# Kernel tuning notes

Measured on AMD Instinct MI355X. Metric: run time of the kernel, lower is better.

The kernel has to match this reference:

```python
import jax, jax.numpy as jnp
import numpy as np

B, C, H, W = 64, 128, 32, 32
GROUPS = 32
EPS = 1e-6
SCALE = 0.044194173824159216  # 1/sqrt(512), as hardcoded in the torch module


def setup_inputs() -> dict:
    key = jax.random.key(0)
    ks = jax.random.split(key, 12)
    s = 1.0 / np.sqrt(C)
    return {
        "x": jax.random.normal(ks[0], (B, C, H, W), dtype=jnp.float32),
        "gn_w": jax.random.normal(ks[1], (C,), dtype=jnp.float32) * 0.02 + 1.0,
        "gn_b": jax.random.normal(ks[2], (C,), dtype=jnp.float32) * 0.02,
        "wq": jax.random.uniform(ks[3], (C, C), jnp.float32, -s, s),
        "bq": jax.random.uniform(ks[4], (C,), jnp.float32, -s, s),
        "wk": jax.random.uniform(ks[5], (C, C), jnp.float32, -s, s),
        "bk": jax.random.uniform(ks[6], (C,), jnp.float32, -s, s),
        "wv": jax.random.uniform(ks[7], (C, C), jnp.float32, -s, s),
        "bv": jax.random.uniform(ks[8], (C,), jnp.float32, -s, s),
        "wo": jax.random.uniform(ks[9], (C, C), jnp.float32, -s, s),
        "bo": jax.random.uniform(ks[10], (C,), jnp.float32, -s, s),
    }


def reference(x, gn_w, gn_b, wq, bq, wk, bk, wv, bv, wo, bo):
    b = x.shape[0]
    res = x
    # GroupNorm(32 groups, 128 channels): normalize over (channels_per_group, H, W)
    xg = x.reshape(b, GROUPS, C // GROUPS, H * W)
    mean = xg.mean(axis=(2, 3), keepdims=True)
    var = xg.var(axis=(2, 3), keepdims=True)
    xn = (xg - mean) * jax.lax.rsqrt(var + EPS)
    xn = xn.reshape(b, C, H, W) * gn_w[:, None, None] + gn_b[:, None, None]
    # flatten spatial -> sequence: [b, S=1024, C=128]
    t = xn.reshape(b, C, H * W).transpose(0, 2, 1)
    q = t @ wq.T + bq
    k = t @ wk.T + bk
    v = t @ wv.T + bv
    att = jnp.einsum('bsc,btc->bst', q, k) * SCALE  # [b, S, S]
    att = jax.nn.softmax(att, axis=-1)
    o = jnp.einsum('bst,btc->bsc', att, v)
    o = o @ wo.T + bo
    out = o.transpose(0, 2, 1).reshape(b, C, H, W) + res
    return out
```

## Files before the change

kernel.cpp:

```cpp
#include <hip/hip_runtime.h>
#include <hip/hip_bf16.h>

#define BATCH 64
#define CCH 128
#define SEQ 1024
#define NG 32
#define EPSV 1e-6f
#define SCALEV 0.044194173824159216f
#define QPRE (0.044194173824159216f * 1.4426950408889634f)

typedef short v8s __attribute__((ext_vector_type(8)));
typedef short v4s __attribute__((ext_vector_type(4)));
typedef float v4f __attribute__((ext_vector_type(4)));
typedef int   v4i __attribute__((ext_vector_type(4)));
typedef unsigned short us;

__device__ __forceinline__ us f2bf(float f) {
    __hip_bfloat16 h = __float2bfloat16(f);
    return *reinterpret_cast<us*>(&h);
}

__device__ __forceinline__ int cvtpk(float lo, float hi) {
    int r;
    asm("v_cvt_pk_bf16_f32 %0, %1, %2" : "=v"(r) : "v"(lo), "v"(hi));
    return r;
}

#if __has_builtin(__builtin_amdgcn_exp2f)
#define EXP2F(x) __builtin_amdgcn_exp2f(x)
#else
#define EXP2F(x) exp2f(x)
#endif

#define MFMA16(a, b, c) __builtin_amdgcn_mfma_f32_16x16x32_bf16(a, b, c, 0, 0, 0)

__device__ __forceinline__ void gld_lds16(const us* g, us* l) {
    __builtin_amdgcn_global_load_lds(
        (const __attribute__((address_space(1))) void*)g,
        (__attribute__((address_space(3))) void*)l, 16, 0, 0);
}

__global__ void prep_gn(const float* __restrict__ wq, const float* __restrict__ wk,
                        const float* __restrict__ wv, const float* __restrict__ wo,
                        us* wbf, const float* __restrict__ x,
                        float* meanr, float* rstdr) {
    int tid = threadIdx.x;
    if (blockIdx.x < 256) {
        int i = blockIdx.x * 256 + tid;
        const float* srcs[4] = {wq, wk, wv, wo};
        wbf[i] = f2bf(srcs[i >> 14][i & 16383]);
        return;
    }
    int bg = blockIdx.x - 256;
    const float4* p = (const float4*)(x + (size_t)bg * (4 * SEQ));
    float s1 = 0.f, s2 = 0.f;
    #pragma unroll
    for (int i = 0; i < 4; i++) {
        float4 v = p[i * 256 + tid];
        s1 += v.x + v.y + v.z + v.w;
        s2 += v.x * v.x + v.y * v.y + v.z * v.z + v.w * v.w;
    }
    #pragma unroll
    for (int off = 32; off; off >>= 1) {
        s1 += __shfl_down(s1, off);
        s2 += __shfl_down(s2, off);
    }
    __shared__ float a1[4], a2[4];
    int w = tid >> 6, l = tid & 63;
    if (l == 0) { a1[w] = s1; a2[w] = s2; }
    __syncthreads();
    if (tid == 0) {
        float t1 = a1[0] + a1[1] + a1[2] + a1[3];
        float t2 = a2[0] + a2[1] + a2[2] + a2[3];
        float mean = t1 * (1.0f / (4 * SEQ));
        float var  = t2 * (1.0f / (4 * SEQ)) - mean * mean;
        meanr[bg] = mean;
        rstdr[bg] = rsqrtf(var + EPSV);
    }
}

__global__ __launch_bounds__(256, 4) void qkv_kernel(
    const float* __restrict__ x, const float* __restrict__ gn_w,
    const float* __restrict__ gn_b, const float* __restrict__ meanr,
    const float* __restrict__ rstdr, const us* __restrict__ wbf,
    const float* __restrict__ bq, const float* __restrict__ bk,
    const float* __restrict__ bv,
    us* Q, us* K, us* Vt)
{
    __shared__ us tls[64 * 136];
    __shared__ float sa[CCH], sb[CCH];
    int b  = blockIdx.x >> 4;
    int s0 = (blockIdx.x & 15) * 64;
    int tid = threadIdx.x;
    const float* xb = x + (size_t)b * CCH * SEQ;

    if (tid < CCH) {
        int g = tid >> 2;
        float rs = rstdr[b * NG + g];
        float mu = meanr[b * NG + g];
        float a_ = rs * gn_w[tid];
        sa[tid] = a_;
        sb[tid] = gn_b[tid] - mu * a_;
    }
    __syncthreads();

    #pragma unroll
    for (int rep = 0; rep < 8; rep++) {
        int idx = rep * 256 + tid;
        int c = idx >> 4, s4 = idx & 15;
        float4 v = *(const float4*)&xb[c * SEQ + s0 + s4 * 4];
        float a_ = sa[c], b_ = sb[c];
        int sbase = s4 * 4;
        tls[(sbase + 0) * 136 + c] = f2bf(v.x * a_ + b_);
        tls[(sbase + 1) * 136 + c] = f2bf(v.y * a_ + b_);
        tls[(sbase + 2) * 136 + c] = f2bf(v.z * a_ + b_);
        tls[(sbase + 3) * 136 + c] = f2bf(v.w * a_ + b_);
    }
    __syncthreads();

    int w = tid >> 6, lane = tid & 63;
    int m = lane & 15, quad = lane >> 4;

    v8s a[4][4];
    #pragma unroll
    for (int st = 0; st < 4; st++)
        #pragma unroll
        for (int ch = 0; ch < 4; ch++)
            a[st][ch] = *(const v8s*)&tls[(st * 16 + m) * 136 + ch * 32 + quad * 8];

    us* Qb = Q + (size_t)b * SEQ * CCH;
    us* Kb = K + (size_t)b * SEQ * CCH;
    us* Vb = Vt + (size_t)b * CCH * SEQ;

    #pragma unroll
    for (int t = 0; t < 6; t++) {
        int T = w * 6 + t;
        int o = T >> 3, ct = T & 7;
        int col = ct * 16 + m;
        const us* wmat = wbf + o * 16384;
        v8s bfr[4];
        #pragma unroll
        for (int ch = 0; ch < 4; ch++)
            bfr[ch] = *(const v8s*)&wmat[(ct * 16 + m) * 128 + ch * 32 + quad * 8];
        const float* bb = (o == 0) ? bq : (o == 1) ? bk : bv;
        float bias = bb[col];

        #pragma unroll
        for (int st = 0; st < 4; st++) {
            v4f acc = {0,0,0,0};
            #pragma unroll
            for (int ch = 0; ch < 4; ch++)
                acc = MFMA16(a[st][ch], bfr[ch], acc);
            int srow = s0 + st * 16 + quad * 4;
            if (o == 0) {
                #pragma unroll
                for (int r = 0; r < 4; r++)
                    Qb[(size_t)(srow + r) * 128 + col] = f2bf((acc[r] + bias) * QPRE);
            } else if (o == 1) {
                #pragma unroll
                for (int r = 0; r < 4; r++)
                    Kb[(size_t)(srow + r) * 128 + col] = f2bf(acc[r] + bias);
            } else {
                v4s pk;
                #pragma unroll
                for (int r = 0; r < 4; r++) pk[r] = (short)f2bf(acc[r] + bias);
                *(v4s*)&Vb[(size_t)col * SEQ + srow] = pk;
            }
        }
    }
}

__global__ __launch_bounds__(256, 2) void attn_kernel(
    const us* __restrict__ Q, const us* __restrict__ K,
    const us* __restrict__ Vt, const us* __restrict__ wbo,
    const float* __restrict__ bo, const float* __restrict__ x,
    float* __restrict__ out)
{
    __shared__ char smem_raw[65536];

    int i = blockIdx.x;
    int b  = (i & 7) * 8 + ((i >> 3) & 7);
    int qt = i >> 6;
    int tid = threadIdx.x;
    int w = tid >> 6, lane = tid & 63;
    int m = lane & 15, quad = lane >> 4;
    int qrow0 = qt * 128 + w * 32;
    const us* Qb = Q + (size_t)b * SEQ * CCH;
    const us* Kb = K + (size_t)b * SEQ * CCH;
    const us* Vb = Vt + (size_t)b * CCH * SEQ;

    v8s aq[2][4];
    #pragma unroll
    for (int st = 0; st < 2; st++)
        #pragma unroll
        for (int ch = 0; ch < 4; ch++)
            aq[st][ch] = *(const v8s*)&Qb[(size_t)(qrow0 + st * 16 + m) * 128 + ch * 32 + quad * 8];

    v4f oacc[2][8];
    #pragma unroll
    for (int st = 0; st < 2; st++)
        #pragma unroll
        for (int ct = 0; ct < 8; ct++) oacc[st][ct] = (v4f){0, 0, 0, 0};
    float lrun[2] = {0.f, 0.f};

    const us* kg[4]; const us* vg[4];
    int jb = w * 4;
    #pragma unroll
    for (int j4 = 0; j4 < 4; j4++) {
        int j = jb + j4;
        int kr = 4 * j + (lane >> 4);
        kg[j4] = Kb + (size_t)kr * 128 + ((lane & 15) ^ (kr & 15)) * 8;
        int vc = 8 * j + (lane >> 3);
        vg[j4] = Vb + (size_t)vc * SEQ + ((lane & 7) ^ (vc & 7)) * 8;
    }
    int idx0 = 2 * (quad & 1) * 16 + m;
    int idx1 = idx0 + 16;

    #pragma unroll
    for (int j4 = 0; j4 < 4; j4++) {
        gld_lds16(kg[j4], (us*)smem_raw + (jb + j4) * 512);
        gld_lds16(vg[j4], (us*)(smem_raw + 16384) + (jb + j4) * 512);
    }

    for (int kt = 0; kt < 16; kt++) {
        int boff  = (kt & 1) ? 32768 : 0;
        int boffn = boff ^ 32768;
        __builtin_amdgcn_s_barrier();
        if (kt < 15) {
            #pragma unroll
            for (int j4 = 0; j4 < 4; j4++) {
                gld_lds16(kg[j4] + (size_t)(kt + 1) * 8192,
                          (us*)(smem_raw + boffn) + (jb + j4) * 512);
                gld_lds16(vg[j4] + (size_t)(kt + 1) * 64,
                          (us*)(smem_raw + boffn + 16384) + (jb + j4) * 512);
            }
            asm volatile("s_waitcnt vmcnt(8)" ::: "memory");
        } else {
            asm volatile("s_waitcnt vmcnt(0)" ::: "memory");
        }
        __builtin_amdgcn_s_barrier();

        const us* kl = (const us*)(smem_raw + boff);
        const us* vl = (const us*)(smem_raw + boff + 16384);

        __builtin_amdgcn_s_setprio(1);

        v4f acc0[4], acc1[4];
        int e[2][4][2];

        #define QK_STEP(c2) { \
            int krow = (c2) * 16 + m; \
            v4f A0 = {0,0,0,0}, A1 = {0,0,0,0}; \
            _Pragma("unroll") \
            for (int ch = 0; ch < 4; ch++) { \
                int chunk = (ch * 4 + quad) ^ (krow & 15); \
                v8s kb = *(const v8s*)&kl[krow * 128 + chunk * 8]; \
                A0 = MFMA16(kb, aq[0][ch], A0); \
                A1 = MFMA16(kb, aq[1][ch], A1); \
            } \
            acc0[c2] = A0; acc1[c2] = A1; }

        #define EXP_STEP(c2) { \
            float p0[4], p1[4]; \
            _Pragma("unroll") \
            for (int r = 0; r < 4; r++) { \
                p0[r] = EXP2F(acc0[c2][r]); \
                p1[r] = EXP2F(acc1[c2][r]); \
                lrun[0] += p0[r]; lrun[1] += p1[r]; \
            } \
            e[0][c2][0] = cvtpk(p0[0], p0[1]); e[0][c2][1] = cvtpk(p0[2], p0[3]); \
            e[1][c2][0] = cvtpk(p1[0], p1[1]); e[1][c2][1] = cvtpk(p1[2], p1[3]); }

        QK_STEP(0)
        QK_STEP(1)
        EXP_STEP(0)
        QK_STEP(2)
        EXP_STEP(1)
        QK_STEP(3)
        EXP_STEP(2)
        EXP_STEP(3)

        #define SHFL_STEP(kc2, paw) { \
            _Pragma("unroll") \
            for (int st = 0; st < 2; st++) { \
                int c0 = (quad < 2) ? e[st][2 * (kc2)][0] : e[st][2 * (kc2) + 1][0]; \
                int c1 = (quad < 2) ? e[st][2 * (kc2)][1] : e[st][2 * (kc2) + 1][1]; \
                v4i t; \
                t[0] = __shfl(c0, idx0); \
                t[1] = __shfl(c1, idx0); \
                t[2] = __shfl(c0, idx1); \
                t[3] = __shfl(c1, idx1); \
                paw[st] = __builtin_bit_cast(v8s, t); } }

        v8s pa0[2], pa1[2];
        SHFL_STEP(0, pa0)
        #pragma unroll
        for (int ct = 0; ct < 8; ct++) {
            int vrow = ct * 16 + m;
            int chunk = quad ^ (vrow & 7);
            v8s vb = *(const v8s*)&vl[vrow * 64 + chunk * 8];
            oacc[0][ct] = MFMA16(pa0[0], vb, oacc[0][ct]);
            oacc[1][ct] = MFMA16(pa0[1], vb, oacc[1][ct]);
        }
        SHFL_STEP(1, pa1)
        #pragma unroll
        for (int ct = 0; ct < 8; ct++) {
            int vrow = ct * 16 + m;
            int chunk = (4 + quad) ^ (vrow & 7);
            v8s vb = *(const v8s*)&vl[vrow * 64 + chunk * 8];
            oacc[0][ct] = MFMA16(pa1[0], vb, oacc[0][ct]);
            oacc[1][ct] = MFMA16(pa1[1], vb, oacc[1][ct]);
        }
        __builtin_amdgcn_s_setprio(0);
        #undef QK_STEP
        #undef EXP_STEP
        #undef SHFL_STEP
    }

    float inv[2][4];
    #pragma unroll
    for (int st = 0; st < 2; st++) {
        float rs = lrun[st];
        rs += __shfl_xor(rs, 16);
        rs += __shfl_xor(rs, 32);
        #pragma unroll
        for (int r = 0; r < 4; r++)
            inv[st][r] = 1.0f / __shfl(rs, quad * 4 + r);
    }
    __syncthreads();
    us* olds = (us*)smem_raw;
    #pragma unroll
    for (int st = 0; st < 2; st++)
        #pragma unroll
        for (int ct = 0; ct < 8; ct++)
            #pragma unroll
            for (int r = 0; r < 4; r++)
                olds[(w * 32 + st * 16 + quad * 4 + r) * 136 + ct * 16 + m] =
                    f2bf(oacc[st][ct][r] * inv[st][r]);
    __syncthreads();

    const float* xb = x + (size_t)b * CCH * SEQ;
    float* ob = out + (size_t)b * CCH * SEQ;
    int sbase = qt * 128 + w * 32;
    v8s obf[2][4];
    #pragma unroll
    for (int st = 0; st < 2; st++)
        #pragma unroll
        for (int ch = 0; ch < 4; ch++)
            obf[st][ch] = *(const v8s*)&olds[(w * 32 + st * 16 + m) * 136 + ch * 32 + quad * 8];
    #pragma unroll
    for (int mt = 0; mt < 8; mt++) {
        v8s af[4];
        #pragma unroll
        for (int ch = 0; ch < 4; ch++)
            af[ch] = *(const v8s*)&wbo[(mt * 16 + m) * 128 + ch * 32 + quad * 8];
        #pragma unroll
        for (int st = 0; st < 2; st++) {
            v4f acc = {0,0,0,0};
            #pragma unroll
            for (int ch = 0; ch < 4; ch++)
                acc = MFMA16(af[ch], obf[st][ch], acc);
            #pragma unroll
            for (int r = 0; r < 4; r++) {
                int c = mt * 16 + quad * 4 + r;
                int idx = c * SEQ + sbase + st * 16 + m;
                ob[idx] = acc[r] + bo[c] + xb[idx];
            }
        }
    }
}

extern "C" void kernel_launch(void* const* d_in, const int* in_sizes, int n_in,
                              void* d_out, int out_size, void* d_ws, size_t ws_size,
                              hipStream_t stream) {
    const float* x    = (const float*)d_in[0];
    const float* gn_w = (const float*)d_in[1];
    const float* gn_b = (const float*)d_in[2];
    const float* wq   = (const float*)d_in[3];
    const float* bq   = (const float*)d_in[4];
    const float* wk   = (const float*)d_in[5];
    const float* bk   = (const float*)d_in[6];
    const float* wv   = (const float*)d_in[7];
    const float* bv   = (const float*)d_in[8];
    const float* wo   = (const float*)d_in[9];
    const float* bo   = (const float*)d_in[10];
    float* out = (float*)d_out;

    char* ws = (char*)d_ws;
    us* wbf      = (us*)ws;
    float* meanr = (float*)(ws + 131072);
    float* rstdr = (float*)(ws + 139264);
    us* Qbuf     = (us*)(ws + 147456);
    us* Kbuf     = (us*)(ws + 147456 + 16777216ull);
    us* Vtbuf    = (us*)(ws + 147456 + 2ull * 16777216ull);

    prep_gn<<<256 + BATCH * NG, 256, 0, stream>>>(wq, wk, wv, wo, wbf, x, meanr, rstdr);
    qkv_kernel<<<1024, 256, 0, stream>>>(x, gn_w, gn_b, meanr, rstdr, wbf,
                                         bq, bk, bv, Qbuf, Kbuf, Vtbuf);
    attn_kernel<<<512, 256, 0, stream>>>(Qbuf, Kbuf, Vtbuf, wbf + 3 * 16384,
                                         bo, x, out);
}
```

Baseline: 168.1 us.

## Stage QKV outputs through LDS for coalesced stores; single-buffer V to raise attention occupancy

The QKV projection now writes its bf16 results into shared memory per output matrix and then stores them to global memory as coalesced 16-byte vectors, replacing scattered 2-byte stores. The attention kernel keeps K double-buffered but gives V a single 16KB buffer, reloaded after a barrier once the PV step finishes. This drops LDS to 48KB so launch bounds can request 3 blocks per CU. The trade-off is an extra barrier per key tile and less overlap on the V load, which is now exposed to latency.

```diff
diff --git a/kernel.cpp b/kernel.cpp
--- a/kernel.cpp
+++ b/kernel.cpp
@@ -87,7 +87,7 @@
     const float* __restrict__ bv,
     us* Q, us* K, us* Vt)
 {
-    __shared__ us tls[64 * 136];
+    __shared__ us tls[9216];
     __shared__ float sa[CCH], sb[CCH];
     int b  = blockIdx.x >> 4;
     int s0 = (blockIdx.x & 15) * 64;
@@ -127,56 +127,76 @@
         #pragma unroll
         for (int ch = 0; ch < 4; ch++)
             a[st][ch] = *(const v8s*)&tls[(st * 16 + m) * 136 + ch * 32 + quad * 8];
+    __syncthreads();
 
     us* Qb = Q + (size_t)b * SEQ * CCH;
     us* Kb = K + (size_t)b * SEQ * CCH;
     us* Vb = Vt + (size_t)b * CCH * SEQ;
 
     #pragma unroll
-    for (int t = 0; t < 6; t++) {
-        int T = w * 6 + t;
-        int o = T >> 3, ct = T & 7;
-        int col = ct * 16 + m;
+    for (int o = 0; o < 3; o++) {
         const us* wmat = wbf + o * 16384;
-        v8s bfr[4];
-        #pragma unroll
-        for (int ch = 0; ch < 4; ch++)
-            bfr[ch] = *(const v8s*)&wmat[(ct * 16 + m) * 128 + ch * 32 + quad * 8];
         const float* bb = (o == 0) ? bq : (o == 1) ? bk : bv;
-        float bias = bb[col];
-
-        #pragma unroll
-        for (int st = 0; st < 4; st++) {
-            v4f acc = {0,0,0,0};
+        #pragma unroll
+        for (int t2 = 0; t2 < 2; t2++) {
+            int T = (o * 2 + t2) * 4 + w;
+            int ct = T & 7;
+            int col = ct * 16 + m;
+            v8s bfr[4];
             #pragma unroll
             for (int ch = 0; ch < 4; ch++)
-                acc = MFMA16(a[st][ch], bfr[ch], acc);
-            int srow = s0 + st * 16 + quad * 4;
-            if (o == 0) {
+                bfr[ch] = *(const v8s*)&wmat[(ct * 16 + m) * 128 + ch * 32 + quad * 8];
+            float bias = bb[col];
+            #pragma unroll
+            for (int st = 0; st < 4; st++) {
+                v4f acc = {0,0,0,0};
                 #pragma unroll
-                for (int r = 0; r < 4; r++)
-                    Qb[(size_t)(srow + r) * 128 + col] = f2bf((acc[r] + bias) * QPRE);
-            } else if (o == 1) {
-                #pragma unroll
-                for (int r = 0; r < 4; r++)
-                    Kb[(size_t)(srow + r) * 128 + col] = f2bf(acc[r] + bias);
-            } else {
-                v4s pk;
-                #pragma unroll
-                for (int r = 0; r < 4; r++) pk[r] = (short)f2bf(acc[r] + bias);
-                *(v4s*)&Vb[(size_t)col * SEQ + srow] = pk;
+                for (int ch = 0; ch < 4; ch++)
+                    acc = MFMA16(a[st][ch], bfr[ch], acc);
+                if (o < 2) {
+                    #pragma unroll
+                    for (int r = 0; r < 4; r++) {
+                        float v = acc[r] + bias;
+                        if (o == 0) v *= QPRE;
+                        tls[(st * 16 + quad * 4 + r) * 136 + col] = f2bf(v);
+                    }
+                } else {
+                    #pragma unroll
+                    for (int r = 0; r < 4; r++)
+                        tls[col * 72 + st * 16 + quad * 4 + r] = f2bf(acc[r] + bias);
+                }
             }
         }
-    }
-}
-
-__global__ __launch_bounds__(256, 2) void attn_kernel(
+        __syncthreads();
+        if (o < 2) {
+            us* dst = (o == 0) ? Qb : Kb;
+            #pragma unroll
+            for (int rep = 0; rep < 4; rep++) {
+                int idx = rep * 256 + tid;
+                int row = idx >> 4, c8 = idx & 15;
+                *(v8s*)&dst[(size_t)(s0 + row) * 128 + c8 * 8] =
+                    *(const v8s*)&tls[row * 136 + c8 * 8];
+            }
+        } else {
+            #pragma unroll
+            for (int rep = 0; rep < 4; rep++) {
+                int idx = rep * 256 + tid;
+                int c = idx >> 3, c8 = idx & 7;
+                *(v8s*)&Vb[(size_t)c * SEQ + s0 + c8 * 8] =
+                    *(const v8s*)&tls[c * 72 + c8 * 8];
+            }
+        }
+        if (o < 2) __syncthreads();
+    }
+}
+
+__global__ __launch_bounds__(256, 3) void attn_kernel(
     const us* __restrict__ Q, const us* __restrict__ K,
     const us* __restrict__ Vt, const us* __restrict__ wbo,
     const float* __restrict__ bo, const float* __restrict__ x,
     float* __restrict__ out)
 {
-    __shared__ char smem_raw[65536];
+    __shared__ char smem_raw[49152];
 
     int i = blockIdx.x;
     int b  = (i & 7) * 8 + ((i >> 3) & 7);
@@ -219,29 +239,24 @@
     #pragma unroll
     for (int j4 = 0; j4 < 4; j4++) {
         gld_lds16(kg[j4], (us*)smem_raw + (jb + j4) * 512);
-        gld_lds16(vg[j4], (us*)(smem_raw + 16384) + (jb + j4) * 512);
+        gld_lds16(vg[j4], (us*)(smem_raw + 32768) + (jb + j4) * 512);
     }
 
     for (int kt = 0; kt < 16; kt++) {
-        int boff  = (kt & 1) ? 32768 : 0;
-        int boffn = boff ^ 32768;
-        __builtin_amdgcn_s_barrier();
+        int kcur = (kt & 1) ? 16384 : 0;
         if (kt < 15) {
             #pragma unroll
-            for (int j4 = 0; j4 < 4; j4++) {
+            for (int j4 = 0; j4 < 4; j4++)
                 gld_lds16(kg[j4] + (size_t)(kt + 1) * 8192,
-                          (us*)(smem_raw + boffn) + (jb + j4) * 512);
-                gld_lds16(vg[j4] + (size_t)(kt + 1) * 64,
-                          (us*)(smem_raw + boffn + 16384) + (jb + j4) * 512);
-            }
-            asm volatile("s_waitcnt vmcnt(8)" ::: "memory");
+                          (us*)(smem_raw + (kcur ^ 16384)) + (jb + j4) * 512);
+            asm volatile("s_waitcnt vmcnt(4)" ::: "memory");
         } else {
             asm volatile("s_waitcnt vmcnt(0)" ::: "memory");
         }
         __builtin_amdgcn_s_barrier();
 
-        const us* kl = (const us*)(smem_raw + boff);
-        const us* vl = (const us*)(smem_raw + boff + 16384);
+        const us* kl = (const us*)(smem_raw + kcur);
+        const us* vl = (const us*)(smem_raw + 32768);
 
         __builtin_amdgcn_s_setprio(1);
 
@@ -315,6 +330,14 @@
         #undef QK_STEP
         #undef EXP_STEP
         #undef SHFL_STEP
+
+        __builtin_amdgcn_s_barrier();
+        if (kt < 15) {
+            #pragma unroll
+            for (int j4 = 0; j4 < 4; j4++)
+                gld_lds16(vg[j4] + (size_t)(kt + 1) * 64,
+                          (us*)(smem_raw + 32768) + (jb + j4) * 512);
+        }
     }
 
     float inv[2][4];
```

After: 187.6 us. 11.6% more time.
